# Kernel tuning notes

Hardware: AMD Instinct MI355X
Metric: run time of the kernel (lower is better)

## Reference

```python
import jax, jax.numpy as jnp
import numpy as np

T = 0.15
ALPHA = 1.0
EPS = 1e-8  # torch.cosine_similarity eps


def setup_inputs() -> dict:
    key = jax.random.key(0)
    k1, k2 = jax.random.split(key)
    x = jax.random.normal(k1, (4096, 1024), dtype=jnp.float32)
    y = jax.random.normal(k2, (4096, 1024), dtype=jnp.float32)
    return {"x": x, "y": y}


def reference(x, y):
    N = x.shape[0]
    nx = jnp.linalg.norm(x, axis=1)  # [N]
    ny = jnp.linalg.norm(y, axis=1)  # [N]

    # positive pairs: cos(x_i, y_i)/T -> exp
    pos = jnp.exp(jnp.sum(x * y, axis=1) / jnp.maximum(nx * ny, EPS) / T)  # [N]

    # pairwise exp-cosine matrices via GEMM (replaces N^2 python loop)
    Sxx = jnp.exp((x @ x.T) / jnp.maximum(nx[:, None] * nx[None, :], EPS) / T)
    Sxy = jnp.exp((x @ y.T) / jnp.maximum(nx[:, None] * ny[None, :], EPS) / T)

    mask = 1.0 - jnp.eye(N, dtype=x.dtype)  # i != j only
    row_sums = jnp.sum((Sxx + Sxy) * mask, axis=1)  # [N]
    # FAITHFUL to source bug: accumulator `sum` never reset across i -> cumulative
    neg = jnp.cumsum(row_sums)  # [N]

    nce_loss = -jnp.sum(jnp.log(pos / neg))

    # JS divergence with batchmean KL (torch KLDivLoss(log_mean, target))
    a = jax.nn.softmax(x, axis=1)
    b = jax.nn.softmax(y, axis=1)
    log_mean = jnp.log((a + b) * 0.5)
    kl_a = jnp.sum(a * (jnp.log(a) - log_mean)) / N
    kl_b = jnp.sum(b * (jnp.log(b) - log_mean)) / N
    js_loss = (kl_a + kl_b) * 0.5

    loss = nce_loss + ALPHA * js_loss
    return loss.reshape(1)
```

## Files before the change

### kernel.cpp

```cpp
#include <hip/hip_runtime.h>
#include <stdint.h>

#define N_ROWS 4096
#define D_DIM  1024
#define ROWB   1024
#define T_TEMP 0.15f

#define AS1 __attribute__((address_space(1)))
#define AS3 __attribute__((address_space(3)))

typedef float f32x4  __attribute__((ext_vector_type(4)));
typedef int   i32x4v __attribute__((ext_vector_type(4)));

__device__ __forceinline__ float wsum(float v) {
#pragma unroll
  for (int m = 32; m >= 1; m >>= 1) v += __shfl_xor(v, m, 64);
  return v;
}
__device__ __forceinline__ float wmax(float v) {
#pragma unroll
  for (int m = 32; m >= 1; m >>= 1) v = fmaxf(v, __shfl_xor(v, m, 64));
  return v;
}

__global__ __launch_bounds__(256) void prep_kernel(
    const float* __restrict__ x, const float* __restrict__ y,
    unsigned char* __restrict__ Bb, float* __restrict__ inv_n,
    float* __restrict__ logpos, float* __restrict__ js,
    float* __restrict__ rowsum) {
  if (threadIdx.x < 4) rowsum[blockIdx.x * 4 + threadIdx.x] = 0.0f;

  const int wid = threadIdx.x >> 6, lane = threadIdx.x & 63;
  const int row = blockIdx.x * 4 + wid;
  const float4* xp = (const float4*)(x + (size_t)row * D_DIM) + lane * 4;
  const float4* yp = (const float4*)(y + (size_t)row * D_DIM) + lane * 4;

  float xv[16], yv[16];
#pragma unroll
  for (int i = 0; i < 4; ++i) {
    float4 a = xp[i], b = yp[i];
    xv[i*4+0]=a.x; xv[i*4+1]=a.y; xv[i*4+2]=a.z; xv[i*4+3]=a.w;
    yv[i*4+0]=b.x; yv[i*4+1]=b.y; yv[i*4+2]=b.z; yv[i*4+3]=b.w;
  }

  float sx2=0.f, sy2=0.f, sxy=0.f, mx=-1e30f, my=-1e30f;
#pragma unroll
  for (int k = 0; k < 16; ++k) {
    sx2 = fmaf(xv[k], xv[k], sx2);
    sy2 = fmaf(yv[k], yv[k], sy2);
    sxy = fmaf(xv[k], yv[k], sxy);
    mx = fmaxf(mx, xv[k]); my = fmaxf(my, yv[k]);
  }
  sx2 = wsum(sx2); sy2 = wsum(sy2); sxy = wsum(sxy);
  mx = wmax(mx);  my = wmax(my);

  float ex[16], ey[16], sex=0.f, sey=0.f;
#pragma unroll
  for (int k = 0; k < 16; ++k) {
    ex[k] = __expf(xv[k] - mx); ey[k] = __expf(yv[k] - my);
    sex += ex[k]; sey += ey[k];
  }
  sex = wsum(sex); sey = wsum(sey);
  const float lsex = __logf(sex), lsey = __logf(sey);
  const float rsex = 1.f / sex,  rsey = 1.f / sey;

  float term = 0.f;
#pragma unroll
  for (int k = 0; k < 16; ++k) {
    float a = ex[k] * rsex, b = ey[k] * rsey;
    float lm = __logf(0.5f * (a + b));
    term += a * ((xv[k] - mx - lsex) - lm) + b * ((yv[k] - my - lsey) - lm);
  }
  term = wsum(term);

  if (lane == 0) {
    const float nx = sqrtf(sx2), ny = sqrtf(sy2);
    inv_n[row] = 1.f / nx;
    inv_n[N_ROWS + row] = 1.f / ny;
    logpos[row] = sxy / fmaxf(nx * ny, 1e-8f) / T_TEMP;
    js[row] = term;
  }

  int p[4], q[4];
#pragma unroll
  for (int w = 0; w < 4; ++w) {
    int v = 0;
    v = __builtin_amdgcn_cvt_pk_fp8_f32(xv[w*4+0], xv[w*4+1], v, false);
    v = __builtin_amdgcn_cvt_pk_fp8_f32(xv[w*4+2], xv[w*4+3], v, true);
    p[w] = v;
    int u = 0;
    u = __builtin_amdgcn_cvt_pk_fp8_f32(yv[w*4+0], yv[w*4+1], u, false);
    u = __builtin_amdgcn_cvt_pk_fp8_f32(yv[w*4+2], yv[w*4+3], u, true);
    q[w] = u;
  }
  const int ktp = lane >> 2;
  const int lq  = lane & 3;
  const int kkb = lq >> 1;
  const int h0  = (lq & 1) * 2;
  {
    char* ob = (char*)Bb + (size_t)row * ROWB + ktp * 64 + kkb * 8 + h0 * 16;
    *(int2*)(ob)      = make_int2(p[0], p[1]);
    *(int2*)(ob + 16) = make_int2(p[2], p[3]);
    char* oy = (char*)Bb + (size_t)(N_ROWS + row) * ROWB + ktp * 64 + kkb * 8 + h0 * 16;
    *(int2*)(oy)      = make_int2(q[0], q[1]);
    *(int2*)(oy + 16) = make_int2(q[2], q[3]);
  }
}

#define GLL(src, dst) __builtin_amdgcn_global_load_lds((const AS1 void*)(src), (AS3 void*)(dst), 16, 0, 0)
#define SBAR __builtin_amdgcn_sched_barrier(0)

__global__ __launch_bounds__(256, 3) void gemm_fused(
    const unsigned char* __restrict__ Bb, const float* __restrict__ inv_n,
    float* __restrict__ rowsum) {
  __shared__ __align__(16) char As[2 * 8192];
  __shared__ __align__(16) char Bs[2 * 8192];
  const int tid = threadIdx.x;
  const int wid = tid >> 6, lane = tid & 63;
  const int lo = lane & 15, hi = lane >> 4;

  int bi, bj;
  bool sym = false;
  {
    const int idx = blockIdx.x;
    if (idx < 1024) {
      bi = idx >> 5; bj = 32 + (idx & 31);
    } else {
      const int t = idx - 1024;
      int b = (int)((65.0 - sqrt((double)(4225 - 8 * t))) * 0.5);
      while ((b + 1) * (65 - (b + 1)) / 2 <= t) ++b;
      while (b * (65 - b) / 2 > t) --b;
      bi = b;
      bj = b + (t - b * (65 - b) / 2);
      sym = (bi != bj);
    }
  }
  const int grow0 = bi * 128;
  const int gcol0 = bj * 128;
  const int wrow = (wid >> 1) * 64, wcol = (wid & 1) * 64;

  f32x4 acc[4][4] = {};

  const int sr = tid >> 2;
  const int sh = (tid & 3) ^ ((tid >> 3) & 3);
  const char* gA = (const char*)Bb + (size_t)(grow0 + sr) * ROWB + sh * 16;
  const char* gB = (const char*)Bb + (size_t)(gcol0 + sr) * ROWB + sh * 16;

#define STG(kt_, b_) do { \
    GLL(gA + (size_t)(kt_) * 64,                      As + (b_) * 8192 + tid * 16); \
    GLL(gA + 64 * (size_t)ROWB + (size_t)(kt_) * 64,  As + (b_) * 8192 + 4096 + tid * 16); \
    GLL(gB + (size_t)(kt_) * 64,                      Bs + (b_) * 8192 + tid * 16); \
    GLL(gB + 64 * (size_t)ROWB + (size_t)(kt_) * 64,  Bs + (b_) * 8192 + 4096 + tid * 16); \
  } while (0)

  const int xr = (lo >> 1) & 3;
  const int rslot = (hi ^ xr) * 16;

  union U { i32x4v v; long l[2]; };

#define RD_FRAGS(b_) do { _Pragma("unroll") \
    for (int m = 0; m < 4; ++m) \
      a[m].v = *(const i32x4v*)(As + (b_) * 8192 + (wrow + m * 16 + lo) * 64 + rslot); \
    _Pragma("unroll") \
    for (int n = 0; n < 4; ++n) \
      bv[n].v = *(const i32x4v*)(Bs + (b_) * 8192 + (wcol + n * 16 + lo) * 64 + rslot); \
  } while (0)

#define MFMA32 do { _Pragma("unroll") \
    for (int n = 0; n < 4; ++n) \
      _Pragma("unroll") \
      for (int m = 0; m < 4; ++m) { \
        acc[m][n] = __builtin_amdgcn_mfma_f32_16x16x32_fp8_fp8( \
            a[m].l[0], bv[n].l[0], acc[m][n], 0, 0, 0); \
        acc[m][n] = __builtin_amdgcn_mfma_f32_16x16x32_fp8_fp8( \
            a[m].l[1], bv[n].l[1], acc[m][n], 0, 0, 0); \
      } \
  } while (0)

  STG(0, 0);
  asm volatile("s_waitcnt vmcnt(0)" ::: "memory");
  __builtin_amdgcn_s_barrier();

  U a[4], bv[4];
#pragma unroll 1
  for (int kt = 0; kt < 15; ++kt) {
    const int b = kt & 1;
    RD_FRAGS(b);
    SBAR;
    STG(kt + 1, b ^ 1);
    asm volatile("s_waitcnt lgkmcnt(0)" ::: "memory");
    SBAR;
    __builtin_amdgcn_s_setprio(1);
    MFMA32;
    __builtin_amdgcn_s_setprio(0);
    SBAR;
    asm volatile("s_waitcnt vmcnt(0)" ::: "memory");
    __builtin_amdgcn_s_barrier();
  }
  RD_FRAGS(1);
  asm volatile("s_waitcnt lgkmcnt(0)" ::: "memory");
  SBAR;
  MFMA32;

  const float C = 1.4426950408889634f / T_TEMP;
  float invc[4], invr[4][4];
#pragma unroll
  for (int n = 0; n < 4; ++n)
    invc[n] = inv_n[gcol0 + wcol + n * 16 + lo] * C;
#pragma unroll
  for (int m = 0; m < 4; ++m)
#pragma unroll
    for (int r = 0; r < 4; ++r)
      invr[m][r] = inv_n[grow0 + wrow + m * 16 + hi * 4 + r];

  float rp[4][4] = {};
  float cp[4] = {};
#pragma unroll
  for (int m = 0; m < 4; ++m)
#pragma unroll
    for (int n = 0; n < 4; ++n)
#pragma unroll
      for (int r = 0; r < 4; ++r) {
        const int i = grow0 + wrow + m * 16 + hi * 4 + r;
        const int j = gcol0 + wcol + n * 16 + lo;
        float e2 = exp2f(acc[m][n][r] * invr[m][r] * invc[n]);
        if (j == i || j == i + N_ROWS) e2 = 0.0f;
        rp[m][r] += e2;
        cp[n] += e2;
      }

#pragma unroll
  for (int m = 0; m < 4; ++m)
#pragma unroll
    for (int r = 0; r < 4; ++r) {
      float v = rp[m][r];
      v += __shfl_xor(v, 1, 16);
      v += __shfl_xor(v, 2, 16);
      v += __shfl_xor(v, 4, 16);
      v += __shfl_xor(v, 8, 16);
      if (lo == 0)
        atomicAdd(&rowsum[grow0 + wrow + m * 16 + hi * 4 + r], v);
    }

  if (sym) {
#pragma unroll
    for (int n = 0; n < 4; ++n) {
      float v = cp[n];
      v += __shfl_xor(v, 16, 64);
      v += __shfl_xor(v, 32, 64);
      if (hi == 0)
        atomicAdd(&rowsum[gcol0 + wcol + n * 16 + lo], v);
    }
  }
#undef STG
#undef RD_FRAGS
#undef MFMA32
}

__global__ __launch_bounds__(256) void final_kernel(
    const float* __restrict__ rowsum, const float* __restrict__ logpos,
    const float* __restrict__ js, float* __restrict__ out) {
  __shared__ float scan[256];
  __shared__ double ds[4];
  __shared__ float fs[4];
  const int tid = threadIdx.x;
  float loc[16];
  float run = 0.f, jl = 0.f;
#pragma unroll
  for (int k = 0; k < 16; ++k) {
    loc[k] = rowsum[tid * 16 + k];
    run += loc[k];
    jl += js[tid * 16 + k];
  }
  scan[tid] = run;
  __syncthreads();
  for (int d = 1; d < 256; d <<= 1) {
    float add = (tid >= d) ? scan[tid - d] : 0.0f;
    __syncthreads();
    scan[tid] += add;
    __syncthreads();
  }
  float c = scan[tid] - run;
  double acc = 0.0;
#pragma unroll
  for (int k = 0; k < 16; ++k) {
    c += loc[k];
    acc += (double)(logf(c) - logpos[tid * 16 + k]);
  }
#pragma unroll
  for (int m = 32; m >= 1; m >>= 1) {
    acc += __shfl_xor(acc, m, 64);
    jl  += __shfl_xor(jl, m, 64);
  }
  if ((tid & 63) == 0) { ds[tid >> 6] = acc; fs[tid >> 6] = jl; }
  __syncthreads();
  if (tid == 0) {
    const double nce = ds[0] + ds[1] + ds[2] + ds[3];
    const double jst = (double)(fs[0] + fs[1] + fs[2] + fs[3]);
    out[0] = (float)(nce + jst / (2.0 * N_ROWS));
  }
}

extern "C" void kernel_launch(void* const* d_in, const int* in_sizes, int n_in,
                              void* d_out, int out_size, void* d_ws, size_t ws_size,
                              hipStream_t stream) {
  const float* x = (const float*)d_in[0];
  const float* y = (const float*)d_in[1];
  float* out = (float*)d_out;

  char* ws = (char*)d_ws;
  unsigned char* Bb = (unsigned char*)ws;
  float* inv_n  = (float*)(ws + (size_t)8 * 1024 * 1024);
  float* logpos = inv_n + 8192;
  float* rowsum = logpos + 4096;
  float* js     = rowsum + 4096;

  prep_kernel<<<N_ROWS / 4, 256, 0, stream>>>(x, y, Bb, inv_n, logpos, js, rowsum);
  gemm_fused<<<1552, 256, 0, stream>>>(Bb, inv_n, rowsum);
  final_kernel<<<1, 256, 0, stream>>>(rowsum, logpos, js, out);
}
```

Measured before the change: 67.06 us.

## Switch pairwise GEMM from fp8 to per-row-scaled int8 MFMA

Quantizes each row of x and y to int8 using a per-row absmax scale and normalizes cosine terms with the norm of the quantized row. The GEMM then uses the i32 16x16x64 int8 MFMA, one instruction per tile instead of two fp8 16x16x32 instructions. The operand layout written by the prep kernel becomes a plain contiguous row layout. This lowers MFMA instruction count and may improve accuracy over fp8, at the cost of extra quantization work in prep and int-to-float conversion in the epilogue.

New measurement: 65.76 us. Within noise of the previous version (-1.9%).

```diff
diff --git a/kernel.cpp b/kernel.cpp
--- a/kernel.cpp
+++ b/kernel.cpp
@@ -9,8 +9,7 @@
 #define AS1 __attribute__((address_space(1)))
 #define AS3 __attribute__((address_space(3)))
 
-typedef float f32x4  __attribute__((ext_vector_type(4)));
-typedef int   i32x4v __attribute__((ext_vector_type(4)));
+typedef int i32x4v __attribute__((ext_vector_type(4)));
 
 __device__ __forceinline__ float wsum(float v) {
 #pragma unroll
@@ -43,16 +42,18 @@
     yv[i*4+0]=b.x; yv[i*4+1]=b.y; yv[i*4+2]=b.z; yv[i*4+3]=b.w;
   }
 
-  float sx2=0.f, sy2=0.f, sxy=0.f, mx=-1e30f, my=-1e30f;
+  float sx2=0.f, sy2=0.f, sxy=0.f, mx=-1e30f, my=-1e30f, ax=0.f, ay=0.f;
 #pragma unroll
   for (int k = 0; k < 16; ++k) {
     sx2 = fmaf(xv[k], xv[k], sx2);
     sy2 = fmaf(yv[k], yv[k], sy2);
     sxy = fmaf(xv[k], yv[k], sxy);
     mx = fmaxf(mx, xv[k]); my = fmaxf(my, yv[k]);
+    ax = fmaxf(ax, fabsf(xv[k])); ay = fmaxf(ay, fabsf(yv[k]));
   }
   sx2 = wsum(sx2); sy2 = wsum(sy2); sxy = wsum(sxy);
   mx = wmax(mx);  my = wmax(my);
+  ax = wmax(ax);  ay = wmax(ay);
 
   float ex[16], ey[16], sex=0.f, sey=0.f;
 #pragma unroll
@@ -73,10 +74,22 @@
   }
   term = wsum(term);
 
+  const float sxq = 127.0f / ax, syq = 127.0f / ay;
+  int qx[16], qy[16];
+  float q2x = 0.f, q2y = 0.f;
+#pragma unroll
+  for (int k = 0; k < 16; ++k) {
+    qx[k] = (int)rintf(xv[k] * sxq);
+    qy[k] = (int)rintf(yv[k] * syq);
+    q2x += (float)(qx[k] * qx[k]);
+    q2y += (float)(qy[k] * qy[k]);
+  }
+  q2x = wsum(q2x); q2y = wsum(q2y);
+
   if (lane == 0) {
     const float nx = sqrtf(sx2), ny = sqrtf(sy2);
-    inv_n[row] = 1.f / nx;
-    inv_n[N_ROWS + row] = 1.f / ny;
+    inv_n[row] = rsqrtf(q2x);
+    inv_n[N_ROWS + row] = rsqrtf(q2y);
     logpos[row] = sxy / fmaxf(nx * ny, 1e-8f) / T_TEMP;
     js[row] = term;
   }
@@ -84,27 +97,13 @@
   int p[4], q[4];
 #pragma unroll
   for (int w = 0; w < 4; ++w) {
-    int v = 0;
-    v = __builtin_amdgcn_cvt_pk_fp8_f32(xv[w*4+0], xv[w*4+1], v, false);
-    v = __builtin_amdgcn_cvt_pk_fp8_f32(xv[w*4+2], xv[w*4+3], v, true);
-    p[w] = v;
-    int u = 0;
-    u = __builtin_amdgcn_cvt_pk_fp8_f32(yv[w*4+0], yv[w*4+1], u, false);
-    u = __builtin_amdgcn_cvt_pk_fp8_f32(yv[w*4+2], yv[w*4+3], u, true);
-    q[w] = u;
-  }
-  const int ktp = lane >> 2;
-  const int lq  = lane & 3;
-  const int kkb = lq >> 1;
-  const int h0  = (lq & 1) * 2;
-  {
-    char* ob = (char*)Bb + (size_t)row * ROWB + ktp * 64 + kkb * 8 + h0 * 16;
-    *(int2*)(ob)      = make_int2(p[0], p[1]);
-    *(int2*)(ob + 16) = make_int2(p[2], p[3]);
-    char* oy = (char*)Bb + (size_t)(N_ROWS + row) * ROWB + ktp * 64 + kkb * 8 + h0 * 16;
-    *(int2*)(oy)      = make_int2(q[0], q[1]);
-    *(int2*)(oy + 16) = make_int2(q[2], q[3]);
-  }
+    p[w] = (qx[4*w] & 255) | ((qx[4*w+1] & 255) << 8) |
+           ((qx[4*w+2] & 255) << 16) | ((qx[4*w+3] & 255) << 24);
+    q[w] = (qy[4*w] & 255) | ((qy[4*w+1] & 255) << 8) |
+           ((qy[4*w+2] & 255) << 16) | ((qy[4*w+3] & 255) << 24);
+  }
+  *(int4*)(Bb + (size_t)row * ROWB + lane * 16) = make_int4(p[0], p[1], p[2], p[3]);
+  *(int4*)(Bb + (size_t)(N_ROWS + row) * ROWB + lane * 16) = make_int4(q[0], q[1], q[2], q[3]);
 }
 
 #define GLL(src, dst) __builtin_amdgcn_global_load_lds((const AS1 void*)(src), (AS3 void*)(dst), 16, 0, 0)
@@ -139,7 +138,7 @@
   const int gcol0 = bj * 128;
   const int wrow = (wid >> 1) * 64, wcol = (wid & 1) * 64;
 
-  f32x4 acc[4][4] = {};
+  i32x4v acc[4][4] = {};
 
   const int sr = tid >> 2;
   const int sh = (tid & 3) ^ ((tid >> 3) & 3);
@@ -156,32 +155,28 @@
   const int xr = (lo >> 1) & 3;
   const int rslot = (hi ^ xr) * 16;
 
-  union U { i32x4v v; long l[2]; };
+  i32x4v a[4], bv[4];
 
 #define RD_FRAGS(b_) do { _Pragma("unroll") \
     for (int m = 0; m < 4; ++m) \
-      a[m].v = *(const i32x4v*)(As + (b_) * 8192 + (wrow + m * 16 + lo) * 64 + rslot); \
+      a[m] = *(const i32x4v*)(As + (b_) * 8192 + (wrow + m * 16 + lo) * 64 + rslot); \
     _Pragma("unroll") \
     for (int n = 0; n < 4; ++n) \
-      bv[n].v = *(const i32x4v*)(Bs + (b_) * 8192 + (wcol + n * 16 + lo) * 64 + rslot); \
+      bv[n] = *(const i32x4v*)(Bs + (b_) * 8192 + (wcol + n * 16 + lo) * 64 + rslot); \
   } while (0)
 
-#define MFMA32 do { _Pragma("unroll") \
+#define MFMA16 do { _Pragma("unroll") \
     for (int n = 0; n < 4; ++n) \
       _Pragma("unroll") \
-      for (int m = 0; m < 4; ++m) { \
-        acc[m][n] = __builtin_amdgcn_mfma_f32_16x16x32_fp8_fp8( \
-            a[m].l[0], bv[n].l[0], acc[m][n], 0, 0, 0); \
-        acc[m][n] = __builtin_amdgcn_mfma_f32_16x16x32_fp8_fp8( \
-            a[m].l[1], bv[n].l[1], acc[m][n], 0, 0, 0); \
-      } \
+      for (int m = 0; m < 4; ++m) \
+        acc[m][n] = __builtin_amdgcn_mfma_i32_16x16x64_i8( \
+            a[m], bv[n], acc[m][n], 0, 0, 0); \
   } while (0)
 
   STG(0, 0);
   asm volatile("s_waitcnt vmcnt(0)" ::: "memory");
   __builtin_amdgcn_s_barrier();
 
-  U a[4], bv[4];
 #pragma unroll 1
   for (int kt = 0; kt < 15; ++kt) {
     const int b = kt & 1;
@@ -191,7 +186,7 @@
     asm volatile("s_waitcnt lgkmcnt(0)" ::: "memory");
     SBAR;
     __builtin_amdgcn_s_setprio(1);
-    MFMA32;
+    MFMA16;
     __builtin_amdgcn_s_setprio(0);
     SBAR;
     asm volatile("s_waitcnt vmcnt(0)" ::: "memory");
@@ -200,7 +195,7 @@
   RD_FRAGS(1);
   asm volatile("s_waitcnt lgkmcnt(0)" ::: "memory");
   SBAR;
-  MFMA32;
+  MFMA16;
 
   const float C = 1.4426950408889634f / T_TEMP;
   float invc[4], invr[4][4];
@@ -223,7 +218,7 @@
       for (int r = 0; r < 4; ++r) {
         const int i = grow0 + wrow + m * 16 + hi * 4 + r;
         const int j = gcol0 + wcol + n * 16 + lo;
-        float e2 = exp2f(acc[m][n][r] * invr[m][r] * invc[n]);
+        float e2 = exp2f((float)acc[m][n][r] * invr[m][r] * invc[n]);
         if (j == i || j == i + N_ROWS) e2 = 0.0f;
         rp[m][r] += e2;
         cp[n] += e2;
@@ -254,7 +249,7 @@
   }
 #undef STG
 #undef RD_FRAGS
-#undef MFMA32
+#undef MFMA16
 }
 
 __global__ __launch_bounds__(256) void final_kernel(
```
